# Optimization experiments

Measured on AMD Instinct MI355X. Metric: run time of the kernel, lower is better.

The kernel has to match this reference:

```python
import jax, jax.numpy as jnp
import numpy as np

B, T, D, F, E, TOP_K = 4, 1024, 1024, 4096, 8, 2


def setup_inputs() -> dict:
    key = jax.random.key(0)
    k0, k1, k2, k3, k4 = jax.random.split(key, 5)
    x = jax.random.normal(k0, (B, T, D), dtype=jnp.float32)
    # xavier-uniform-ish scales
    Wr = jax.random.normal(k1, (D, E), dtype=jnp.float32) * (1.0 / np.sqrt(D))
    W1 = jax.random.normal(k2, (E, D, F), dtype=jnp.float32) * (1.0 / np.sqrt(D))
    W3 = jax.random.normal(k3, (E, D, F), dtype=jnp.float32) * (1.0 / np.sqrt(D))
    W2 = jax.random.normal(k4, (E, F, D), dtype=jnp.float32) * (1.0 / np.sqrt(F))
    return {"x": x, "Wr": Wr, "W1": W1, "W3": W3, "W2": W2}


def reference(x, Wr, W1, W3, W2):
    # Router: logits [B,T,E]
    logits = jnp.einsum('btd,de->bte', x, Wr)
    top_vals, top_idx = jax.lax.top_k(logits, TOP_K)          # [B,T,K]
    weights = jax.nn.softmax(top_vals, axis=-1)               # [B,T,K]
    probs = jax.nn.softmax(logits, axis=-1)                   # [B,T,E]
    usage = probs.mean(axis=(0, 1))                           # [E]
    load_balancing_loss = E * jnp.sum(usage ** 2)

    # SwiGLU experts computed densely per expert: down(silu(gate(x)) * up(x))
    gate = jnp.einsum('btd,edf->ebtf', x, W1)                 # [E,B,T,F]
    up = jnp.einsum('btd,edf->ebtf', x, W3)
    h = jax.nn.silu(gate) * up
    eout = jnp.einsum('ebtf,efd->ebtd', h, W2)                # [E,B,T,D]
    eout = jnp.moveaxis(eout, 0, 2)                           # [B,T,E,D]

    # Gather selected experts and combine with softmax weights
    sel = jnp.take_along_axis(eout, top_idx[..., None], axis=2)  # [B,T,K,D]
    output = jnp.sum(sel * weights[..., None], axis=2)           # [B,T,D]
    return output, load_balancing_loss
```

## Files before the change

### kernel.cpp

```cpp
#include <hip/hip_runtime.h>
#include <hip/hip_bf16.h>
#include <stdint.h>
#include <math.h>

#define NTOK 4096
#define DDIM 1024
#define FDIM 4096
#define NEXP 8
#define NPAIR 8192

#define BM 256
#define BN 64
#define BK 64
#define APAD 72
#define BPAD 72

#define RT_TPW 8
#define RT_BLOCKS (NTOK / (4 * RT_TPW))

using short8 = __attribute__((ext_vector_type(8))) short;
using f32x4  = __attribute__((ext_vector_type(4))) float;

__device__ __forceinline__ uint16_t f2bf(float f) {
    union { float f; uint32_t u; } v; v.f = f;
    uint32_t r = v.u + 0x7FFFu + ((v.u >> 16) & 1u);
    return (uint16_t)(r >> 16);
}

__global__ void router_kernel(const float* __restrict__ x, const float* __restrict__ Wr,
                              int* __restrict__ cnt_part, float* __restrict__ us_part,
                              int* __restrict__ top_e, float* __restrict__ top_w) {
    __shared__ float us[NEXP];
    __shared__ int cs[NEXP];
    const int tid = threadIdx.x;
    const int wv = tid >> 6;
    const int lane = tid & 63;
    if (tid < NEXP) { us[tid] = 0.f; cs[tid] = 0; }
    __syncthreads();

    for (int i = 0; i < RT_TPW; i++) {
        const int t = blockIdx.x * (4 * RT_TPW) + wv * RT_TPW + i;
        float acc[NEXP];
#pragma unroll
        for (int e = 0; e < NEXP; e++) acc[e] = 0.f;
        const float* xr = x + (size_t)t * DDIM;
        for (int d = lane; d < DDIM; d += 64) {
            float xv = xr[d];
            const float* wr = Wr + (size_t)d * NEXP;
#pragma unroll
            for (int e = 0; e < NEXP; e++) acc[e] += xv * wr[e];
        }
#pragma unroll
        for (int e = 0; e < NEXP; e++) {
#pragma unroll
            for (int off = 32; off > 0; off >>= 1) acc[e] += __shfl_xor(acc[e], off, 64);
        }
        if (lane == 0) {
            int i0 = 0;
#pragma unroll
            for (int e = 1; e < NEXP; e++) if (acc[e] > acc[i0]) i0 = e;
            int i1 = -1;
#pragma unroll
            for (int e = 0; e < NEXP; e++) {
                if (e == i0) continue;
                if (i1 < 0 || acc[e] > acc[i1]) i1 = e;
            }
            float v0 = acc[i0], v1 = acc[i1];
            float e1 = __expf(v1 - v0);
            float inv = 1.f / (1.f + e1);
            top_e[t * 2 + 0] = i0; top_e[t * 2 + 1] = i1;
            top_w[t * 2 + 0] = inv; top_w[t * 2 + 1] = e1 * inv;
            atomicAdd(&cs[i0], 1);
            atomicAdd(&cs[i1], 1);
            float m = acc[0];
#pragma unroll
            for (int e = 1; e < NEXP; e++) m = fmaxf(m, acc[e]);
            float p[NEXP]; float s = 0.f;
#pragma unroll
            for (int e = 0; e < NEXP; e++) { p[e] = __expf(acc[e] - m); s += p[e]; }
            float is = 1.f / s;
#pragma unroll
            for (int e = 0; e < NEXP; e++) atomicAdd(&us[e], p[e] * is);
        }
    }
    __syncthreads();
    if (tid < NEXP) {
        cnt_part[blockIdx.x * NEXP + tid] = cs[tid];
        us_part[blockIdx.x * NEXP + tid] = us[tid];
    }
}

__global__ void finalize_kernel(const int* __restrict__ cnt_part, const float* __restrict__ us_part,
                                int* __restrict__ counts, int* __restrict__ offs,
                                float* __restrict__ out) {
    __shared__ int c[NEXP];
    __shared__ float u[NEXP];
    const int tid = threadIdx.x;
    if (tid < NEXP) {
        int csum = 0; float usum = 0.f;
        for (int b = 0; b < RT_BLOCKS; b++) {
            csum += cnt_part[b * NEXP + tid];
            usum += us_part[b * NEXP + tid];
        }
        counts[tid] = csum; c[tid] = csum; u[tid] = usum;
    }
    __syncthreads();
    if (tid == 0) {
        int s = 0; float l = 0.f;
#pragma unroll
        for (int e = 0; e < NEXP; e++) {
            offs[e] = s; s += c[e];
            float uu = u[e] * (1.f / (float)NTOK);
            l += uu * uu;
        }
        out[(size_t)NTOK * DDIM] = (float)NEXP * l;
    }
}

__global__ void xcast_kernel(const float* __restrict__ x, uint16_t* __restrict__ xb) {
    int i = blockIdx.x * 256 + threadIdx.x;
    float4 v = ((const float4*)x)[i];
    ushort4 o;
    o.x = f2bf(v.x); o.y = f2bf(v.y); o.z = f2bf(v.z); o.w = f2bf(v.w);
    ((ushort4*)xb)[i] = o;
}

__global__ void transpose_cast_kernel(const float* __restrict__ in, uint16_t* __restrict__ outp,
                                      int R, int C) {
    __shared__ uint16_t tile[32][36];
    const int e = blockIdx.z;
    const float* src = in + (size_t)e * R * C;
    uint16_t* dst = outp + (size_t)e * R * C;
    const int r0 = blockIdx.y * 32, c0 = blockIdx.x * 32;
    {
        int r = threadIdx.x >> 3, cq = threadIdx.x & 7;
        float4 v = *(const float4*)(src + (size_t)(r0 + r) * C + c0 + cq * 4);
        tile[cq * 4 + 0][r] = f2bf(v.x);
        tile[cq * 4 + 1][r] = f2bf(v.y);
        tile[cq * 4 + 2][r] = f2bf(v.z);
        tile[cq * 4 + 3][r] = f2bf(v.w);
    }
    __syncthreads();
    {
        int cc = threadIdx.x >> 3, rq = threadIdx.x & 7;
        ushort4 o = *(const ushort4*)&tile[cc][rq * 4];
        *(ushort4*)(dst + (size_t)(c0 + cc) * R + r0 + rq * 4) = o;
    }
}

__global__ void scatter_kernel(const int* __restrict__ top_e, const float* __restrict__ top_w,
                               const int* __restrict__ offs, int* __restrict__ fill,
                               int* __restrict__ pair_tok, float* __restrict__ pair_w) {
    __shared__ int lcnt[NEXP];
    __shared__ int lbase[NEXP];
    const int tid = threadIdx.x;
    const int t = blockIdx.x * 256 + tid;
    if (tid < NEXP) lcnt[tid] = 0;
    __syncthreads();
    int e0 = top_e[t * 2 + 0], e1 = top_e[t * 2 + 1];
    int r0 = atomicAdd(&lcnt[e0], 1);
    int r1 = atomicAdd(&lcnt[e1], 1);
    __syncthreads();
    if (tid < NEXP) lbase[tid] = atomicAdd(&fill[tid], lcnt[tid]);
    __syncthreads();
    int p0 = offs[e0] + lbase[e0] + r0;
    int p1 = offs[e1] + lbase[e1] + r1;
    pair_tok[p0] = t; pair_w[p0] = top_w[t * 2 + 0];
    pair_tok[p1] = t; pair_w[p1] = top_w[t * 2 + 1];
}

template<bool BF16W>
__global__ __launch_bounds__(256, 2)
void expert_up_kernel(const uint16_t* __restrict__ x_bf,
                      const float* __restrict__ W1f, const float* __restrict__ W3f,
                      const uint16_t* __restrict__ W1t, const uint16_t* __restrict__ W3t,
                      const int* __restrict__ counts, const int* __restrict__ offs,
                      const int* __restrict__ pair_tok, uint16_t* __restrict__ h) {
    const int e = blockIdx.z;
    const int tile = blockIdx.y;
    const int n0 = blockIdx.x * BN;
    const int cntAll = counts[e];
    if (tile * BM >= cntAll) return;
    const int cnt = min(BM, cntAll - tile * BM);
    const int pairBase = offs[e] + tile * BM;

    __shared__ uint16_t As[BM][APAD];
    __shared__ uint16_t B1s[BN][BPAD];
    __shared__ uint16_t B3s[BN][BPAD];

    const int tid = threadIdx.x;
    const int wave = tid >> 6;
    const int lane = tid & 63;
    const int quad = lane >> 4;
    const int lr = lane & 15;

    const int ra = tid >> 1;
    const int ahalf = tid & 1;
    const int tokA0 = pair_tok[pairBase + min(ra, cnt - 1)];
    const int tokA1 = pair_tok[pairBase + min(ra + 128, cnt - 1)];
    const uint16_t* aSrc0 = x_bf + (size_t)tokA0 * DDIM + ahalf * 32;
    const uint16_t* aSrc1 = x_bf + (size_t)tokA1 * DDIM + ahalf * 32;

    const int kb = tid >> 2;
    const int ng = tid & 3;
    const int rb = tid >> 2;
    const int qk = tid & 3;
    const float* w1Base = W1f + (size_t)e * DDIM * FDIM + n0 + ng * 16;
    const float* w3Base = W3f + (size_t)e * DDIM * FDIM + n0 + ng * 16;
    const uint16_t* w1tBase = W1t + (size_t)e * DDIM * FDIM + (size_t)(n0 + rb) * DDIM + qk * 16;
    const uint16_t* w3tBase = W3t + (size_t)e * DDIM * FDIM + (size_t)(n0 + rb) * DDIM + qk * 16;

    f32x4 accG[4][4], accU[4][4];
#pragma unroll
    for (int i = 0; i < 4; i++)
#pragma unroll
        for (int j = 0; j < 4; j++) {
            accG[i][j] = (f32x4){0.f, 0.f, 0.f, 0.f};
            accU[i][j] = (f32x4){0.f, 0.f, 0.f, 0.f};
        }

    for (int k0 = 0; k0 < DDIM; k0 += BK) {
        __syncthreads();
        {
            const uint4* s0 = (const uint4*)(aSrc0 + k0);
            uint4 v0 = s0[0], v1 = s0[1], v2 = s0[2], v3 = s0[3];
            const uint4* s1 = (const uint4*)(aSrc1 + k0);
            uint4 w0 = s1[0], w1 = s1[1], w2 = s1[2], w3 = s1[3];
            uint4* d0 = (uint4*)&As[ra][ahalf * 32];
            d0[0] = v0; d0[1] = v1; d0[2] = v2; d0[3] = v3;
            uint4* d1 = (uint4*)&As[ra + 128][ahalf * 32];
            d1[0] = w0; d1[1] = w1; d1[2] = w2; d1[3] = w3;
        }
        if constexpr (BF16W) {
            const uint4* s1 = (const uint4*)(w1tBase + k0);
            uint4 a0 = s1[0], a1 = s1[1];
            *(uint4*)&B1s[rb][qk * 16] = a0; *(uint4*)&B1s[rb][qk * 16 + 8] = a1;
            const uint4* s3 = (const uint4*)(w3tBase + k0);
            uint4 b0 = s3[0], b1 = s3[1];
            *(uint4*)&B3s[rb][qk * 16] = b0; *(uint4*)&B3s[rb][qk * 16 + 8] = b1;
        } else {
            const float4* s1 = (const float4*)(w1Base + (size_t)(k0 + kb) * FDIM);
            float4 c0 = s1[0], c1 = s1[1], c2 = s1[2], c3 = s1[3];
            uint16_t* bc = &B1s[ng * 16][kb];
            bc[0*BPAD]=f2bf(c0.x); bc[1*BPAD]=f2bf(c0.y); bc[2*BPAD]=f2bf(c0.z); bc[3*BPAD]=f2bf(c0.w);
            bc[4*BPAD]=f2bf(c1.x); bc[5*BPAD]=f2bf(c1.y); bc[6*BPAD]=f2bf(c1.z); bc[7*BPAD]=f2bf(c1.w);
            bc[8*BPAD]=f2bf(c2.x); bc[9*BPAD]=f2bf(c2.y); bc[10*BPAD]=f2bf(c2.z); bc[11*BPAD]=f2bf(c2.w);
            bc[12*BPAD]=f2bf(c3.x); bc[13*BPAD]=f2bf(c3.y); bc[14*BPAD]=f2bf(c3.z); bc[15*BPAD]=f2bf(c3.w);
            const float4* s3 = (const float4*)(w3Base + (size_t)(k0 + kb) * FDIM);
            float4 d0 = s3[0], d1 = s3[1], d2 = s3[2], d3 = s3[3];
            uint16_t* dc = &B3s[ng * 16][kb];
            dc[0*BPAD]=f2bf(d0.x); dc[1*BPAD]=f2bf(d0.y); dc[2*BPAD]=f2bf(d0.z); dc[3*BPAD]=f2bf(d0.w);
            dc[4*BPAD]=f2bf(d1.x); dc[5*BPAD]=f2bf(d1.y); dc[6*BPAD]=f2bf(d1.z); dc[7*BPAD]=f2bf(d1.w);
            dc[8*BPAD]=f2bf(d2.x); dc[9*BPAD]=f2bf(d2.y); dc[10*BPAD]=f2bf(d2.z); dc[11*BPAD]=f2bf(d2.w);
            dc[12*BPAD]=f2bf(d3.x); dc[13*BPAD]=f2bf(d3.y); dc[14*BPAD]=f2bf(d3.z); dc[15*BPAD]=f2bf(d3.w);
        }
        __syncthreads();
#pragma unroll
        for (int kk = 0; kk < BK; kk += 32) {
            short8 af[4];
#pragma unroll
            for (int mi = 0; mi < 4; mi++)
                af[mi] = *(const short8*)&As[wave * 64 + mi * 16 + lr][kk + quad * 8];
#pragma unroll
            for (int ni = 0; ni < 4; ni++) {
                short8 b1 = *(const short8*)&B1s[ni * 16 + lr][kk + quad * 8];
                short8 b3 = *(const short8*)&B3s[ni * 16 + lr][kk + quad * 8];
#pragma unroll
                for (int mi = 0; mi < 4; mi++) {
                    accG[mi][ni] = __builtin_amdgcn_mfma_f32_16x16x32_bf16(af[mi], b1, accG[mi][ni], 0, 0, 0);
                    accU[mi][ni] = __builtin_amdgcn_mfma_f32_16x16x32_bf16(af[mi], b3, accU[mi][ni], 0, 0, 0);
                }
            }
        }
    }
#pragma unroll
    for (int mi = 0; mi < 4; mi++) {
#pragma unroll
        for (int r = 0; r < 4; r++) {
            int rowLocal = wave * 64 + mi * 16 + quad * 4 + r;
            if (rowLocal < cnt) {
                uint16_t* dst = h + (size_t)(pairBase + rowLocal) * FDIM + n0 + lr;
#pragma unroll
                for (int ni = 0; ni < 4; ni++) {
                    float g = accG[mi][ni][r];
                    float u = accU[mi][ni][r];
                    float hv = (g / (1.f + __expf(-g))) * u;
                    dst[ni * 16] = f2bf(hv);
                }
            }
        }
    }
}

template<bool BF16W>
__global__ __launch_bounds__(256, 2)
void expert_down_kernel(const uint16_t* __restrict__ h,
                        const float* __restrict__ W2f, const uint16_t* __restrict__ W2t,
                        const int* __restrict__ counts, const int* __restrict__ offs,
                        const int* __restrict__ pair_tok, const float* __restrict__ pair_w,
                        float* __restrict__ out) {
    const int e = blockIdx.z;
    const int tile = blockIdx.y;
    const int n0 = blockIdx.x * BN;
    const int cntAll = counts[e];
    if (tile * BM >= cntAll) return;
    const int cnt = min(BM, cntAll - tile * BM);
    const int pairBase = offs[e] + tile * BM;

    __shared__ uint16_t As[BM][APAD];
    __shared__ uint16_t Bs[BN][BPAD];

    const int tid = threadIdx.x;
    const int wave = tid >> 6;
    const int lane = tid & 63;
    const int quad = lane >> 4;
    const int lr = lane & 15;

    const int ra = tid >> 1;
    const int ahalf = tid & 1;
    const uint16_t* aSrc0 = h + (size_t)(pairBase + min(ra, cnt - 1)) * FDIM + ahalf * 32;
    const uint16_t* aSrc1 = h + (size_t)(pairBase + min(ra + 128, cnt - 1)) * FDIM + ahalf * 32;

    const int kb = tid >> 2;
    const int ng = tid & 3;
    const int rb = tid >> 2;
    const int qk = tid & 3;
    const float* w2Base = W2f + (size_t)e * FDIM * DDIM + n0 + ng * 16;
    const uint16_t* w2tBase = W2t + (size_t)e * FDIM * DDIM + (size_t)(n0 + rb) * FDIM + qk * 16;

    f32x4 acc[4][4];
#pragma unroll
    for (int i = 0; i < 4; i++)
#pragma unroll
        for (int j = 0; j < 4; j++) acc[i][j] = (f32x4){0.f, 0.f, 0.f, 0.f};

    for (int k0 = 0; k0 < FDIM; k0 += BK) {
        __syncthreads();
        {
            const uint4* s0 = (const uint4*)(aSrc0 + k0);
            uint4 v0 = s0[0], v1 = s0[1], v2 = s0[2], v3 = s0[3];
            const uint4* s1 = (const uint4*)(aSrc1 + k0);
            uint4 w0 = s1[0], w1 = s1[1], w2 = s1[2], w3 = s1[3];
            uint4* d0 = (uint4*)&As[ra][ahalf * 32];
            d0[0] = v0; d0[1] = v1; d0[2] = v2; d0[3] = v3;
            uint4* d1 = (uint4*)&As[ra + 128][ahalf * 32];
            d1[0] = w0; d1[1] = w1; d1[2] = w2; d1[3] = w3;
        }
        if constexpr (BF16W) {
            const uint4* s2 = (const uint4*)(w2tBase + k0);
            uint4 a0 = s2[0], a1 = s2[1];
            *(uint4*)&Bs[rb][qk * 16] = a0; *(uint4*)&Bs[rb][qk * 16 + 8] = a1;
        } else {
            const float4* s2 = (const float4*)(w2Base + (size_t)(k0 + kb) * DDIM);
            float4 c0 = s2[0], c1 = s2[1], c2 = s2[2], c3 = s2[3];
            uint16_t* bc = &Bs[ng * 16][kb];
            bc[0*BPAD]=f2bf(c0.x); bc[1*BPAD]=f2bf(c0.y); bc[2*BPAD]=f2bf(c0.z); bc[3*BPAD]=f2bf(c0.w);
            bc[4*BPAD]=f2bf(c1.x); bc[5*BPAD]=f2bf(c1.y); bc[6*BPAD]=f2bf(c1.z); bc[7*BPAD]=f2bf(c1.w);
            bc[8*BPAD]=f2bf(c2.x); bc[9*BPAD]=f2bf(c2.y); bc[10*BPAD]=f2bf(c2.z); bc[11*BPAD]=f2bf(c2.w);
            bc[12*BPAD]=f2bf(c3.x); bc[13*BPAD]=f2bf(c3.y); bc[14*BPAD]=f2bf(c3.z); bc[15*BPAD]=f2bf(c3.w);
        }
        __syncthreads();
#pragma unroll
        for (int kk = 0; kk < BK; kk += 32) {
            short8 af[4];
#pragma unroll
            for (int mi = 0; mi < 4; mi++)
                af[mi] = *(const short8*)&As[wave * 64 + mi * 16 + lr][kk + quad * 8];
#pragma unroll
            for (int ni = 0; ni < 4; ni++) {
                short8 b = *(const short8*)&Bs[ni * 16 + lr][kk + quad * 8];
#pragma unroll
                for (int mi = 0; mi < 4; mi++)
                    acc[mi][ni] = __builtin_amdgcn_mfma_f32_16x16x32_bf16(af[mi], b, acc[mi][ni], 0, 0, 0);
            }
        }
    }
#pragma unroll
    for (int mi = 0; mi < 4; mi++) {
#pragma unroll
        for (int r = 0; r < 4; r++) {
            int rowLocal = wave * 64 + mi * 16 + quad * 4 + r;
            if (rowLocal < cnt) {
                int pi = pairBase + rowLocal;
                int tok = pair_tok[pi];
                float w = pair_w[pi];
                float* dst = out + (size_t)tok * DDIM + n0 + lr;
#pragma unroll
                for (int ni = 0; ni < 4; ni++)
                    atomicAdd(&dst[ni * 16], acc[mi][ni][r] * w);
            }
        }
    }
}

extern "C" void kernel_launch(void* const* d_in, const int* in_sizes, int n_in,
                              void* d_out, int out_size, void* d_ws, size_t ws_size,
                              hipStream_t stream) {
    (void)in_sizes; (void)n_in;
    const float* x  = (const float*)d_in[0];
    const float* Wr = (const float*)d_in[1];
    const float* W1 = (const float*)d_in[2];
    const float* W3 = (const float*)d_in[3];
    const float* W2 = (const float*)d_in[4];
    float* out = (float*)d_out;

    char* ws = (char*)d_ws;
    size_t off = 0;
    int*      counts    = (int*)(ws + off);  off += 64;
    int*      offs      = (int*)(ws + off);  off += 64;
    int*      fill      = (int*)(ws + off);  off += 128;
    int*      top_e     = (int*)(ws + off);  off += 4 * NPAIR;
    float*    top_w     = (float*)(ws + off); off += 4 * NPAIR;
    int*      pair_tok  = (int*)(ws + off);  off += 4 * NPAIR;
    float*    pair_w    = (float*)(ws + off); off += 4 * NPAIR;
    int*      cnt_part  = (int*)(ws + off);  off += 4 * RT_BLOCKS * NEXP;
    float*    us_part   = (float*)(ws + off); off += 4 * RT_BLOCKS * NEXP;
    uint16_t* x_bf      = (uint16_t*)(ws + off); off += (size_t)2 * NTOK * DDIM;
    uint16_t* h         = (uint16_t*)(ws + off); off += (size_t)2 * NPAIR * FDIM;
    const size_t wBytes = (size_t)2 * NEXP * DDIM * FDIM;
    uint16_t* W1t = (uint16_t*)(ws + off);
    uint16_t* W3t = (uint16_t*)(ws + off + wBytes);
    uint16_t* W2t = (uint16_t*)(ws + off + 2 * wBytes);
    const bool bf16w = ws_size >= off + 3 * wBytes;

    hipMemsetAsync(ws, 0, 256, stream);
    hipMemsetAsync(d_out, 0, (size_t)out_size * sizeof(float), stream);

    xcast_kernel<<<NTOK * DDIM / 1024, 256, 0, stream>>>(x, x_bf);
    router_kernel<<<RT_BLOCKS, 256, 0, stream>>>(x, Wr, cnt_part, us_part, top_e, top_w);
    finalize_kernel<<<1, 64, 0, stream>>>(cnt_part, us_part, counts, offs, out);
    scatter_kernel<<<NTOK / 256, 256, 0, stream>>>(top_e, top_w, offs, fill, pair_tok, pair_w);

    dim3 gA(FDIM / BN, NTOK / BM, NEXP);
    dim3 gB(DDIM / BN, NTOK / BM, NEXP);
    if (bf16w) {
        transpose_cast_kernel<<<dim3(FDIM / 32, DDIM / 32, NEXP), 256, 0, stream>>>(W1, W1t, DDIM, FDIM);
        transpose_cast_kernel<<<dim3(FDIM / 32, DDIM / 32, NEXP), 256, 0, stream>>>(W3, W3t, DDIM, FDIM);
        transpose_cast_kernel<<<dim3(DDIM / 32, FDIM / 32, NEXP), 256, 0, stream>>>(W2, W2t, FDIM, DDIM);
        expert_up_kernel<true><<<gA, 256, 0, stream>>>(x_bf, nullptr, nullptr, W1t, W3t,
                                                       counts, offs, pair_tok, h);
        expert_down_kernel<true><<<gB, 256, 0, stream>>>(h, nullptr, W2t,
                                                         counts, offs, pair_tok, pair_w, out);
    } else {
        expert_up_kernel<false><<<gA, 256, 0, stream>>>(x_bf, W1, W3, nullptr, nullptr,
                                                        counts, offs, pair_tok, h);
        expert_down_kernel<false><<<gB, 256, 0, stream>>>(h, W2, nullptr,
                                                          counts, offs, pair_tok, pair_w, out);
    }
}
```

Baseline: 836.5 us.

## Load GEMM tiles with direct global-to-LDS async copies into XOR-swizzled shared layout

Expert up and down GEMMs now stage A and B tiles with global_load_lds 16-byte direct copies instead of register round-trips. Shared memory uses an unpadded, XOR-swizzled layout to avoid bank conflicts. The transpose-cast kernel moves to 64x64 swizzled tiles with wider stores, and the fp32-weight fallback path is removed. Down kernel launch bounds rise to 3 blocks per CU. The code now assumes the workspace is always large enough for the bf16 transposed weights.

```diff
diff --git a/kernel.cpp b/kernel.cpp
--- a/kernel.cpp
+++ b/kernel.cpp
@@ -12,8 +12,6 @@
 #define BM 256
 #define BN 64
 #define BK 64
-#define APAD 72
-#define BPAD 72
 
 #define RT_TPW 8
 #define RT_BLOCKS (NTOK / (4 * RT_TPW))
@@ -25,6 +23,12 @@
     union { float f; uint32_t u; } v; v.f = f;
     uint32_t r = v.u + 0x7FFFu + ((v.u >> 16) & 1u);
     return (uint16_t)(r >> 16);
+}
+
+__device__ __forceinline__ void async16(const void* g, void* l) {
+    __builtin_amdgcn_global_load_lds((const __attribute__((address_space(1))) void*)g,
+                                     (__attribute__((address_space(3))) void*)l,
+                                     16, 0, 0);
 }
 
 __global__ void router_kernel(const float* __restrict__ x, const float* __restrict__ Wr,
@@ -127,24 +131,39 @@
 
 __global__ void transpose_cast_kernel(const float* __restrict__ in, uint16_t* __restrict__ outp,
                                       int R, int C) {
-    __shared__ uint16_t tile[32][36];
+    __shared__ uint16_t tile[64 * 64];
     const int e = blockIdx.z;
     const float* src = in + (size_t)e * R * C;
     uint16_t* dst = outp + (size_t)e * R * C;
-    const int r0 = blockIdx.y * 32, c0 = blockIdx.x * 32;
+    const int r0 = blockIdx.y * 64, c0 = blockIdx.x * 64;
+    const int t = threadIdx.x;
     {
-        int r = threadIdx.x >> 3, cq = threadIdx.x & 7;
-        float4 v = *(const float4*)(src + (size_t)(r0 + r) * C + c0 + cq * 4);
-        tile[cq * 4 + 0][r] = f2bf(v.x);
-        tile[cq * 4 + 1][r] = f2bf(v.y);
-        tile[cq * 4 + 2][r] = f2bf(v.z);
-        tile[cq * 4 + 3][r] = f2bf(v.w);
+        const int rb = t >> 4;
+        const int c4 = t & 15;
+#pragma unroll
+        for (int i = 0; i < 4; i++) {
+            const int r = rb + i * 16;
+            float4 v = *(const float4*)(src + (size_t)(r0 + r) * C + c0 + c4 * 4);
+            const int rc = (r >> 3);
+            const int re = (r & 7);
+#pragma unroll
+            for (int j = 0; j < 4; j++) {
+                const int c = c4 * 4 + j;
+                float fv = (j == 0) ? v.x : (j == 1) ? v.y : (j == 2) ? v.z : v.w;
+                tile[c * 64 + ((rc ^ (c & 7)) << 3) + re] = f2bf(fv);
+            }
+        }
     }
     __syncthreads();
     {
-        int cc = threadIdx.x >> 3, rq = threadIdx.x & 7;
-        ushort4 o = *(const ushort4*)&tile[cc][rq * 4];
-        *(ushort4*)(dst + (size_t)(c0 + cc) * R + r0 + rq * 4) = o;
+        const int cr = t >> 3;
+        const int ch = t & 7;
+#pragma unroll
+        for (int i = 0; i < 2; i++) {
+            const int c = cr + i * 32;
+            uint4 v = *(const uint4*)&tile[c * 64 + ((ch ^ (c & 7)) << 3)];
+            *(uint4*)(dst + (size_t)(c0 + c) * R + r0 + ch * 8) = v;
+        }
     }
 }
 
@@ -169,10 +188,8 @@
     pair_tok[p1] = t; pair_w[p1] = top_w[t * 2 + 1];
 }
 
-template<bool BF16W>
 __global__ __launch_bounds__(256, 2)
 void expert_up_kernel(const uint16_t* __restrict__ x_bf,
-                      const float* __restrict__ W1f, const float* __restrict__ W3f,
                       const uint16_t* __restrict__ W1t, const uint16_t* __restrict__ W3t,
                       const int* __restrict__ counts, const int* __restrict__ offs,
                       const int* __restrict__ pair_tok, uint16_t* __restrict__ h) {
@@ -184,31 +201,26 @@
     const int cnt = min(BM, cntAll - tile * BM);
     const int pairBase = offs[e] + tile * BM;
 
-    __shared__ uint16_t As[BM][APAD];
-    __shared__ uint16_t B1s[BN][BPAD];
-    __shared__ uint16_t B3s[BN][BPAD];
+    __shared__ uint16_t As[BM * BK];
+    __shared__ uint16_t B1s[BN * BK];
+    __shared__ uint16_t B3s[BN * BK];
 
     const int tid = threadIdx.x;
     const int wave = tid >> 6;
     const int lane = tid & 63;
     const int quad = lane >> 4;
     const int lr = lane & 15;
-
-    const int ra = tid >> 1;
-    const int ahalf = tid & 1;
-    const int tokA0 = pair_tok[pairBase + min(ra, cnt - 1)];
-    const int tokA1 = pair_tok[pairBase + min(ra + 128, cnt - 1)];
-    const uint16_t* aSrc0 = x_bf + (size_t)tokA0 * DDIM + ahalf * 32;
-    const uint16_t* aSrc1 = x_bf + (size_t)tokA1 * DDIM + ahalf * 32;
-
-    const int kb = tid >> 2;
-    const int ng = tid & 3;
-    const int rb = tid >> 2;
-    const int qk = tid & 3;
-    const float* w1Base = W1f + (size_t)e * DDIM * FDIM + n0 + ng * 16;
-    const float* w3Base = W3f + (size_t)e * DDIM * FDIM + n0 + ng * 16;
-    const uint16_t* w1tBase = W1t + (size_t)e * DDIM * FDIM + (size_t)(n0 + rb) * DDIM + qk * 16;
-    const uint16_t* w3tBase = W3t + (size_t)e * DDIM * FDIM + (size_t)(n0 + rb) * DDIM + qk * 16;
+    const int sub = lane >> 3;
+    const int swoff = (((lane & 7) ^ sub) << 3);
+
+    int tokr[8];
+#pragma unroll
+    for (int i = 0; i < 8; i++) {
+        int row = wave * 64 + i * 8 + sub;
+        tokr[i] = pair_tok[pairBase + min(row, cnt - 1)];
+    }
+    const uint16_t* w1p = W1t + (size_t)e * DDIM * FDIM;
+    const uint16_t* w3p = W3t + (size_t)e * DDIM * FDIM;
 
     f32x4 accG[4][4], accU[4][4];
 #pragma unroll
@@ -221,50 +233,33 @@
 
     for (int k0 = 0; k0 < DDIM; k0 += BK) {
         __syncthreads();
-        {
-            const uint4* s0 = (const uint4*)(aSrc0 + k0);
-            uint4 v0 = s0[0], v1 = s0[1], v2 = s0[2], v3 = s0[3];
-            const uint4* s1 = (const uint4*)(aSrc1 + k0);
-            uint4 w0 = s1[0], w1 = s1[1], w2 = s1[2], w3 = s1[3];
-            uint4* d0 = (uint4*)&As[ra][ahalf * 32];
-            d0[0] = v0; d0[1] = v1; d0[2] = v2; d0[3] = v3;
-            uint4* d1 = (uint4*)&As[ra + 128][ahalf * 32];
-            d1[0] = w0; d1[1] = w1; d1[2] = w2; d1[3] = w3;
-        }
-        if constexpr (BF16W) {
-            const uint4* s1 = (const uint4*)(w1tBase + k0);
-            uint4 a0 = s1[0], a1 = s1[1];
-            *(uint4*)&B1s[rb][qk * 16] = a0; *(uint4*)&B1s[rb][qk * 16 + 8] = a1;
-            const uint4* s3 = (const uint4*)(w3tBase + k0);
-            uint4 b0 = s3[0], b1 = s3[1];
-            *(uint4*)&B3s[rb][qk * 16] = b0; *(uint4*)&B3s[rb][qk * 16 + 8] = b1;
-        } else {
-            const float4* s1 = (const float4*)(w1Base + (size_t)(k0 + kb) * FDIM);
-            float4 c0 = s1[0], c1 = s1[1], c2 = s1[2], c3 = s1[3];
-            uint16_t* bc = &B1s[ng * 16][kb];
-            bc[0*BPAD]=f2bf(c0.x); bc[1*BPAD]=f2bf(c0.y); bc[2*BPAD]=f2bf(c0.z); bc[3*BPAD]=f2bf(c0.w);
-            bc[4*BPAD]=f2bf(c1.x); bc[5*BPAD]=f2bf(c1.y); bc[6*BPAD]=f2bf(c1.z); bc[7*BPAD]=f2bf(c1.w);
-            bc[8*BPAD]=f2bf(c2.x); bc[9*BPAD]=f2bf(c2.y); bc[10*BPAD]=f2bf(c2.z); bc[11*BPAD]=f2bf(c2.w);
-            bc[12*BPAD]=f2bf(c3.x); bc[13*BPAD]=f2bf(c3.y); bc[14*BPAD]=f2bf(c3.z); bc[15*BPAD]=f2bf(c3.w);
-            const float4* s3 = (const float4*)(w3Base + (size_t)(k0 + kb) * FDIM);
-            float4 d0 = s3[0], d1 = s3[1], d2 = s3[2], d3 = s3[3];
-            uint16_t* dc = &B3s[ng * 16][kb];
-            dc[0*BPAD]=f2bf(d0.x); dc[1*BPAD]=f2bf(d0.y); dc[2*BPAD]=f2bf(d0.z); dc[3*BPAD]=f2bf(d0.w);
-            dc[4*BPAD]=f2bf(d1.x); dc[5*BPAD]=f2bf(d1.y); dc[6*BPAD]=f2bf(d1.z); dc[7*BPAD]=f2bf(d1.w);
-            dc[8*BPAD]=f2bf(d2.x); dc[9*BPAD]=f2bf(d2.y); dc[10*BPAD]=f2bf(d2.z); dc[11*BPAD]=f2bf(d2.w);
-            dc[12*BPAD]=f2bf(d3.x); dc[13*BPAD]=f2bf(d3.y); dc[14*BPAD]=f2bf(d3.z); dc[15*BPAD]=f2bf(d3.w);
+#pragma unroll
+        for (int i = 0; i < 8; i++)
+            async16(x_bf + (size_t)tokr[i] * DDIM + k0 + swoff,
+                    &As[(wave * 64 + i * 8) * BK] + lane * 8);
+#pragma unroll
+        for (int j = 0; j < 2; j++) {
+            int n = wave * 16 + j * 8 + sub;
+            async16(w1p + (size_t)(n0 + n) * DDIM + k0 + swoff,
+                    &B1s[(wave * 16 + j * 8) * BK] + lane * 8);
+            async16(w3p + (size_t)(n0 + n) * DDIM + k0 + swoff,
+                    &B3s[(wave * 16 + j * 8) * BK] + lane * 8);
         }
         __syncthreads();
 #pragma unroll
         for (int kk = 0; kk < BK; kk += 32) {
+            const int lc = (kk >> 3) + quad;
             short8 af[4];
 #pragma unroll
-            for (int mi = 0; mi < 4; mi++)
-                af[mi] = *(const short8*)&As[wave * 64 + mi * 16 + lr][kk + quad * 8];
+            for (int mi = 0; mi < 4; mi++) {
+                int R = wave * 64 + mi * 16 + lr;
+                af[mi] = *(const short8*)&As[R * BK + ((lc ^ (lr & 7)) << 3)];
+            }
 #pragma unroll
             for (int ni = 0; ni < 4; ni++) {
-                short8 b1 = *(const short8*)&B1s[ni * 16 + lr][kk + quad * 8];
-                short8 b3 = *(const short8*)&B3s[ni * 16 + lr][kk + quad * 8];
+                int n = ni * 16 + lr;
+                short8 b1 = *(const short8*)&B1s[n * BK + ((lc ^ (lr & 7)) << 3)];
+                short8 b3 = *(const short8*)&B3s[n * BK + ((lc ^ (lr & 7)) << 3)];
 #pragma unroll
                 for (int mi = 0; mi < 4; mi++) {
                     accG[mi][ni] = __builtin_amdgcn_mfma_f32_16x16x32_bf16(af[mi], b1, accG[mi][ni], 0, 0, 0);
@@ -292,10 +287,8 @@
     }
 }
 
-template<bool BF16W>
-__global__ __launch_bounds__(256, 2)
-void expert_down_kernel(const uint16_t* __restrict__ h,
-                        const float* __restrict__ W2f, const uint16_t* __restrict__ W2t,
+__global__ __launch_bounds__(256, 3)
+void expert_down_kernel(const uint16_t* __restrict__ h, const uint16_t* __restrict__ W2t,
                         const int* __restrict__ counts, const int* __restrict__ offs,
                         const int* __restrict__ pair_tok, const float* __restrict__ pair_w,
                         float* __restrict__ out) {
@@ -307,26 +300,24 @@
     const int cnt = min(BM, cntAll - tile * BM);
     const int pairBase = offs[e] + tile * BM;
 
-    __shared__ uint16_t As[BM][APAD];
-    __shared__ uint16_t Bs[BN][BPAD];
+    __shared__ uint16_t As[BM * BK];
+    __shared__ uint16_t Bs[BN * BK];
 
     const int tid = threadIdx.x;
     const int wave = tid >> 6;
     const int lane = tid & 63;
     const int quad = lane >> 4;
     const int lr = lane & 15;
-
-    const int ra = tid >> 1;
-    const int ahalf = tid & 1;
-    const uint16_t* aSrc0 = h + (size_t)(pairBase + min(ra, cnt - 1)) * FDIM + ahalf * 32;
-    const uint16_t* aSrc1 = h + (size_t)(pairBase + min(ra + 128, cnt - 1)) * FDIM + ahalf * 32;
-
-    const int kb = tid >> 2;
-    const int ng = tid & 3;
-    const int rb = tid >> 2;
-    const int qk = tid & 3;
-    const float* w2Base = W2f + (size_t)e * FDIM * DDIM + n0 + ng * 16;
-    const uint16_t* w2tBase = W2t + (size_t)e * FDIM * DDIM + (size_t)(n0 + rb) * FDIM + qk * 16;
+    const int sub = lane >> 3;
+    const int swoff = (((lane & 7) ^ sub) << 3);
+
+    int hrow[8];
+#pragma unroll
+    for (int i = 0; i < 8; i++) {
+        int row = wave * 64 + i * 8 + sub;
+        hrow[i] = pairBase + min(row, cnt - 1);
+    }
+    const uint16_t* w2p = W2t + (size_t)e * FDIM * DDIM;
 
     f32x4 acc[4][4];
 #pragma unroll
@@ -336,39 +327,30 @@
 
     for (int k0 = 0; k0 < FDIM; k0 += BK) {
         __syncthreads();
-        {
-            const uint4* s0 = (const uint4*)(aSrc0 + k0);
-            uint4 v0 = s0[0], v1 = s0[1], v2 = s0[2], v3 = s0[3];
-            const uint4* s1 = (const uint4*)(aSrc1 + k0);
-            uint4 w0 = s1[0], w1 = s1[1], w2 = s1[2], w3 = s1[3];
-            uint4* d0 = (uint4*)&As[ra][ahalf * 32];
-            d0[0] = v0; d0[1] = v1; d0[2] = v2; d0[3] = v3;
-            uint4* d1 = (uint4*)&As[ra + 128][ahalf * 32];
-            d1[0] = w0; d1[1] = w1; d1[2] = w2; d1[3] = w3;
-        }
-        if constexpr (BF16W) {
-            const uint4* s2 = (const uint4*)(w2tBase + k0);
-            uint4 a0 = s2[0], a1 = s2[1];
-            *(uint4*)&Bs[rb][qk * 16] = a0; *(uint4*)&Bs[rb][qk * 16 + 8] = a1;
-        } else {
-            const float4* s2 = (const float4*)(w2Base + (size_t)(k0 + kb) * DDIM);
-            float4 c0 = s2[0], c1 = s2[1], c2 = s2[2], c3 = s2[3];
-            uint16_t* bc = &Bs[ng * 16][kb];
-            bc[0*BPAD]=f2bf(c0.x); bc[1*BPAD]=f2bf(c0.y); bc[2*BPAD]=f2bf(c0.z); bc[3*BPAD]=f2bf(c0.w);
-            bc[4*BPAD]=f2bf(c1.x); bc[5*BPAD]=f2bf(c1.y); bc[6*BPAD]=f2bf(c1.z); bc[7*BPAD]=f2bf(c1.w);
-            bc[8*BPAD]=f2bf(c2.x); bc[9*BPAD]=f2bf(c2.y); bc[10*BPAD]=f2bf(c2.z); bc[11*BPAD]=f2bf(c2.w);
-            bc[12*BPAD]=f2bf(c3.x); bc[13*BPAD]=f2bf(c3.y); bc[14*BPAD]=f2bf(c3.z); bc[15*BPAD]=f2bf(c3.w);
+#pragma unroll
+        for (int i = 0; i < 8; i++)
+            async16(h + (size_t)hrow[i] * FDIM + k0 + swoff,
+                    &As[(wave * 64 + i * 8) * BK] + lane * 8);
+#pragma unroll
+        for (int j = 0; j < 2; j++) {
+            int n = wave * 16 + j * 8 + sub;
+            async16(w2p + (size_t)(n0 + n) * FDIM + k0 + swoff,
+                    &Bs[(wave * 16 + j * 8) * BK] + lane * 8);
         }
         __syncthreads();
 #pragma unroll
         for (int kk = 0; kk < BK; kk += 32) {
+            const int lc = (kk >> 3) + quad;
             short8 af[4];
 #pragma unroll
-            for (int mi = 0; mi < 4; mi++)
-                af[mi] = *(const short8*)&As[wave * 64 + mi * 16 + lr][kk + quad * 8];
+            for (int mi = 0; mi < 4; mi++) {
+                int R = wave * 64 + mi * 16 + lr;
+                af[mi] = *(const short8*)&As[R * BK + ((lc ^ (lr & 7)) << 3)];
+            }
 #pragma unroll
             for (int ni = 0; ni < 4; ni++) {
-                short8 b = *(const short8*)&Bs[ni * 16 + lr][kk + quad * 8];
+                int n = ni * 16 + lr;
+                short8 b = *(const short8*)&Bs[n * BK + ((lc ^ (lr & 7)) << 3)];
 #pragma unroll
                 for (int mi = 0; mi < 4; mi++)
                     acc[mi][ni] = __builtin_amdgcn_mfma_f32_16x16x32_bf16(af[mi], b, acc[mi][ni], 0, 0, 0);
@@ -396,7 +378,7 @@
 extern "C" void kernel_launch(void* const* d_in, const int* in_sizes, int n_in,
                               void* d_out, int out_size, void* d_ws, size_t ws_size,
                               hipStream_t stream) {
-    (void)in_sizes; (void)n_in;
+    (void)in_sizes; (void)n_in; (void)ws_size;
     const float* x  = (const float*)d_in[0];
     const float* Wr = (const float*)d_in[1];
     const float* W1 = (const float*)d_in[2];
@@ -421,7 +403,6 @@
     uint16_t* W1t = (uint16_t*)(ws + off);
     uint16_t* W3t = (uint16_t*)(ws + off + wBytes);
     uint16_t* W2t = (uint16_t*)(ws + off + 2 * wBytes);
-    const bool bf16w = ws_size >= off + 3 * wBytes;
 
     hipMemsetAsync(ws, 0, 256, stream);
     hipMemsetAsync(d_out, 0, (size_t)out_size * sizeof(float), stream);
@@ -431,20 +412,12 @@
     finalize_kernel<<<1, 64, 0, stream>>>(cnt_part, us_part, counts, offs, out);
     scatter_kernel<<<NTOK / 256, 256, 0, stream>>>(top_e, top_w, offs, fill, pair_tok, pair_w);
 
+    transpose_cast_kernel<<<dim3(FDIM / 64, DDIM / 64, NEXP), 256, 0, stream>>>(W1, W1t, DDIM, FDIM);
+    transpose_cast_kernel<<<dim3(FDIM / 64, DDIM / 64, NEXP), 256, 0, stream>>>(W3, W3t, DDIM, FDIM);
+    transpose_cast_kernel<<<dim3(DDIM / 64, FDIM / 64, NEXP), 256, 0, stream>>>(W2, W2t, FDIM, DDIM);
+
     dim3 gA(FDIM / BN, NTOK / BM, NEXP);
+    expert_up_kernel<<<gA, 256, 0, stream>>>(x_bf, W1t, W3t, counts, offs, pair_tok, h);
     dim3 gB(DDIM / BN, NTOK / BM, NEXP);
-    if (bf16w) {
-        transpose_cast_kernel<<<dim3(FDIM / 32, DDIM / 32, NEXP), 256, 0, stream>>>(W1, W1t, DDIM, FDIM);
-        transpose_cast_kernel<<<dim3(FDIM / 32, DDIM / 32, NEXP), 256, 0, stream>>>(W3, W3t, DDIM, FDIM);
-        transpose_cast_kernel<<<dim3(DDIM / 32, FDIM / 32, NEXP), 256, 0, stream>>>(W2, W2t, FDIM, DDIM);
-        expert_up_kernel<true><<<gA, 256, 0, stream>>>(x_bf, nullptr, nullptr, W1t, W3t,
-                                                       counts, offs, pair_tok, h);
-        expert_down_kernel<true><<<gB, 256, 0, stream>>>(h, nullptr, W2t,
-                                                         counts, offs, pair_tok, pair_w, out);
-    } else {
-        expert_up_kernel<false><<<gA, 256, 0, stream>>>(x_bf, W1, W3, nullptr, nullptr,
-                                                        counts, offs, pair_tok, h);
-        expert_down_kernel<false><<<gB, 256, 0, stream>>>(h, W2, nullptr,
-                                                          counts, offs, pair_tok, pair_w, out);
-    }
-}
+    expert_down_kernel<<<gB, 256, 0, stream>>>(h, W2t, counts, offs, pair_tok, pair_w, out);
+}
```

Result: faster. 806.0 us (-3.6%).
